# Kernel tuning notes

Measured on AMD Instinct MI355X. Metric: run time of the kernel, lower is better.

The kernel has to match this reference:

```python
import jax, jax.numpy as jnp
import numpy as np

COMMITMENT_COST = 0.25


def setup_inputs() -> dict:
    key = jax.random.key(0)
    k1, k2 = jax.random.split(key)
    B, S, D, K = 16, 4096, 256, 4096
    inputs = jax.random.normal(k1, (B, S, D), dtype=jnp.float32)
    # codebook ~ embedding.weight (init scale irrelevant for correctness baseline)
    codebook = jax.random.normal(k2, (K, D), dtype=jnp.float32)
    return {"inputs": inputs, "codebook": codebook}


def reference(inputs, codebook):
    B, S, D = inputs.shape
    flat = inputs.reshape(-1, D)  # (N, D)
    distances = (
        jnp.sum(flat * flat, axis=1, keepdims=True)
        + jnp.sum(codebook * codebook, axis=1)
        - 2.0 * jnp.matmul(flat, codebook.T)
    )
    encoding_indices = jnp.argmin(distances, axis=1)  # (N,)
    quantized = codebook[encoding_indices].reshape(inputs.shape)  # gather
    # commitment loss: beta * mse(inputs, sg(quantized))
    diff = inputs - jax.lax.stop_gradient(quantized)
    commitment_loss = COMMITMENT_COST * jnp.mean(diff * diff)
    # straight-through estimator
    quantized_st = inputs + jax.lax.stop_gradient(quantized - inputs)
    return quantized_st, commitment_loss, encoding_indices
```

## Files before the change

### kernel.cpp

```cpp
#include <hip/hip_runtime.h>
#include <stdint.h>

typedef _Float16 half8 __attribute__((ext_vector_type(8)));
typedef float f32x4 __attribute__((ext_vector_type(4)));

#define DDIM 256
#define KCODES 4096
#define BM 256
#define BN 256
#define NCH 8
#define DELTA 0.02f
#define FLT_BIG 3.4e38f

#define GLOAD_LDS(gsrc, ldst)                                                        \
    __builtin_amdgcn_global_load_lds(                                                \
        (const __attribute__((address_space(1))) void*)(const void*)(gsrc),          \
        (__attribute__((address_space(3))) void*)(void*)(ldst), 16, 0, 0)

__global__ void cvt_hl_kernel(const float* __restrict__ src, half8* __restrict__ dst) {
    int gid = blockIdx.x * 256 + threadIdx.x;
    int q = gid & 3;
    int ch = (gid >> 2) & 7;
    long row = gid >> 5;
    const float* s = src + row * DDIM + ch * 32 + q * 8;
    const float4 f0 = ((const float4*)s)[0];
    const float4 f1 = ((const float4*)s)[1];
    float vv[8] = {f0.x, f0.y, f0.z, f0.w, f1.x, f1.y, f1.z, f1.w};
    half8 hi, lo;
    #pragma unroll
    for (int j = 0; j < 8; ++j) {
        float v = vv[j];
        _Float16 h = (_Float16)v;
        hi[j] = h; lo[j] = (_Float16)(v - (float)h);
    }
    half8* d = dst + ((row * 8 + ch) << 3);
    d[q] = hi;
    d[q + 4] = lo;
}

__global__ void enorm_kernel(const float* __restrict__ cb, float* __restrict__ en, int K) {
    int gid = blockIdx.x * blockDim.x + threadIdx.x;
    int code = gid >> 6;
    int lane = threadIdx.x & 63;
    if (code >= K) return;
    const float4 v = *reinterpret_cast<const float4*>(&cb[(size_t)code * DDIM + lane * 4]);
    float s = v.x * v.x + v.y * v.y + v.z * v.z + v.w * v.w;
    #pragma unroll
    for (int off = 32; off > 0; off >>= 1) s += __shfl_xor(s, off, 64);
    if (lane == 0) en[code] = s;
}

__global__ __launch_bounds__(512, 2)
void vq_mfma_kernel(const half8* x16, const half8* __restrict__ cb16,
                    const float* __restrict__ en, const float* __restrict__ x,
                    const float* __restrict__ cb, float* out,
                    int* __restrict__ list, int* __restrict__ counter,
                    float* __restrict__ loss_accum, int N) {
    __shared__ __align__(16) half8 Abuf[2][BM * 8];
    __shared__ __align__(16) half8 Bbuf[2][BN * 8];
    __shared__ float en_lds[KCODES];
    __shared__ float red_d[4][BM];
    __shared__ float red_d2[4][BM];
    __shared__ int   red_i[4][BM];
    __shared__ int   binfo[BM];
    __shared__ float wsum[8];

    const int tid = threadIdx.x;
    const int lane = tid & 63;
    const int w = tid >> 6;
    const int wr = w >> 2, wc = w & 3;
    const int l15 = lane & 15, l4 = lane >> 4;
    const int brow = blockIdx.x * BM;
    const size_t ND = (size_t)N * DDIM;

    ((float4*)en_lds)[tid] = ((const float4*)en)[tid];
    ((float4*)en_lds)[tid + 512] = ((const float4*)en)[tid + 512];

    const int lrow = lane >> 3;
    const int swz = (lane & 7) ^ lrow;
    const half8* pA0 = x16 + (size_t)(brow + (w     ) * 8 + lrow) * 64 + swz;
    const half8* pA1 = x16 + (size_t)(brow + (w +  8) * 8 + lrow) * 64 + swz;
    const half8* pA2 = x16 + (size_t)(brow + (w + 16) * 8 + lrow) * 64 + swz;
    const half8* pA3 = x16 + (size_t)(brow + (w + 24) * 8 + lrow) * 64 + swz;
    const half8* pB0 = cb16 + (size_t)((w     ) * 8 + lrow) * 64 + swz;
    const half8* pB1 = cb16 + (size_t)((w +  8) * 8 + lrow) * 64 + swz;
    const half8* pB2 = cb16 + (size_t)((w + 16) * 8 + lrow) * 64 + swz;
    const half8* pB3 = cb16 + (size_t)((w + 24) * 8 + lrow) * 64 + swz;

#define STAGE(b_) do {                                      \
        GLOAD_LDS(pA0, &Abuf[b_][(w     ) * 64]);           \
        GLOAD_LDS(pA1, &Abuf[b_][(w +  8) * 64]);           \
        GLOAD_LDS(pA2, &Abuf[b_][(w + 16) * 64]);           \
        GLOAD_LDS(pA3, &Abuf[b_][(w + 24) * 64]);           \
        GLOAD_LDS(pB0, &Bbuf[b_][(w     ) * 64]);           \
        GLOAD_LDS(pB1, &Bbuf[b_][(w +  8) * 64]);           \
        GLOAD_LDS(pB2, &Bbuf[b_][(w + 16) * 64]);           \
        GLOAD_LDS(pB3, &Bbuf[b_][(w + 24) * 64]);           \
    } while (0)

#define ADVANCE(roll_) do {                                 \
        const int dA = (roll_) ? -56 : 8;                   \
        const int dB = (roll_) ? 16328 : 8;                 \
        pA0 += dA; pA1 += dA; pA2 += dA; pA3 += dA;         \
        pB0 += dB; pB1 += dB; pB2 += dB; pB3 += dB;         \
    } while (0)

    const int sw7 = l15 & 7;
    const _Float16* A0 = (const _Float16*)Abuf;
    const _Float16* B0 = A0 + 32768;
    const _Float16* aH = A0 + wr * 8192 + l15 * 64 + ((l4    ) ^ sw7) * 8;
    const _Float16* aL = A0 + wr * 8192 + l15 * 64 + ((l4 + 4) ^ sw7) * 8;
    const _Float16* bH = B0 + wc * 4096 + l15 * 64 + ((l4    ) ^ sw7) * 8;
    const _Float16* bL = B0 + wc * 4096 + l15 * 64 + ((l4 + 4) ^ sw7) * 8;

    STAGE(0); ADVANCE(false);

    float bestv[8], best2v[8];
    int bidv[8];
    #pragma unroll
    for (int i = 0; i < 8; ++i) { bestv[i] = FLT_BIG; best2v[i] = FLT_BIG; bidv[i] = 0; }

    const int code_sub = wc * 64 + l4 * 4;
    f32x4 acc[4][8];

#define TRI(accr, bh_, bl_, ah_, al_) do {                                              \
        accr = __builtin_amdgcn_mfma_f32_16x16x32_f16(bh_, ah_, accr, 0, 0, 0);         \
        accr = __builtin_amdgcn_mfma_f32_16x16x32_f16(bl_, ah_, accr, 0, 0, 0);         \
        accr = __builtin_amdgcn_mfma_f32_16x16x32_f16(bh_, al_, accr, 0, 0, 0);         \
    } while (0)

    for (int it = 0; it < 16; ++it) {
        #pragma unroll
        for (int m = 0; m < 4; ++m)
            #pragma unroll
            for (int n = 0; n < 8; ++n) acc[m][n] = (f32x4){0.f, 0.f, 0.f, 0.f};

        #pragma unroll
        for (int k = 0; k < 8; ++k) {
            __syncthreads();
            if (k != 7) { STAGE((k + 1) & 1); ADVANCE(k == 6); }
            else if (it != 15) { STAGE(0); ADVANCE(false); }
            __builtin_amdgcn_sched_barrier(0);

            const int o = (k & 1) ? 16384 : 0;
            half8 a_h[8], a_l[8];
            #pragma unroll
            for (int n = 0; n < 8; ++n) {
                a_h[n] = *(const half8*)(aH + o + n * 1024);
                a_l[n] = *(const half8*)(aL + o + n * 1024);
            }
            #pragma unroll
            for (int m = 0; m < 4; ++m) {
                half8 bh = *(const half8*)(bH + o + m * 1024);
                half8 bl = *(const half8*)(bL + o + m * 1024);
                __builtin_amdgcn_s_setprio(1);
                #pragma unroll
                for (int n = 0; n < 8; ++n)
                    TRI(acc[m][n], bh, bl, a_h[n], a_l[n]);
                __builtin_amdgcn_s_setprio(0);
            }
        }

        const int c0 = it * BN;
        #pragma unroll
        for (int m = 0; m < 4; ++m) {
            #pragma unroll
            for (int r = 0; r < 4; ++r) {
                int code = c0 + code_sub + m * 16 + r;
                float e = en_lds[code];
                #pragma unroll
                for (int n = 0; n < 8; ++n) {
                    float dist = fmaf(-2.f, acc[m][n][r], e);
                    if (dist < bestv[n]) { best2v[n] = bestv[n]; bestv[n] = dist; bidv[n] = code; }
                    else if (dist < best2v[n]) best2v[n] = dist;
                }
            }
        }
    }
#undef STAGE
#undef ADVANCE
#undef TRI

    #pragma unroll
    for (int n = 0; n < 8; ++n) {
        float d = bestv[n], d2 = best2v[n];
        int ix = bidv[n];
        #pragma unroll
        for (int off = 16; off < 64; off <<= 1) {
            float od = __shfl_xor(d, off, 64);
            float od2 = __shfl_xor(d2, off, 64);
            int oi = __shfl_xor(ix, off, 64);
            if (od < d || (od == d && oi < ix)) { d2 = fminf(d, od2); d = od; ix = oi; }
            else d2 = fminf(d2, od);
        }
        if (l4 == 0) {
            int row = wr * 128 + n * 16 + l15;
            red_d[wc][row] = d;
            red_d2[wc][row] = d2;
            red_i[wc][row] = ix;
        }
    }
    __syncthreads();

    if (tid < BM) {
        float d = red_d[0][tid], d2 = red_d2[0][tid];
        int ix = red_i[0][tid];
        #pragma unroll
        for (int q = 1; q < 4; ++q) {
            float od = red_d[q][tid], od2 = red_d2[q][tid];
            int oi = red_i[q][tid];
            if (od < d || (od == d && oi < ix)) { d2 = fminf(d, od2); d = od; ix = oi; }
            else d2 = fminf(d2, od);
        }
        int fl = (d2 - d < DELTA) ? 1 : 0;
        out[ND + 1 + brow + tid] = (float)ix;
        binfo[tid] = ix | (fl << 16);
        if (fl) {
            int pos = atomicAdd(counter, 1);
            list[pos] = brow + tid;
        }
    }
    __syncthreads();

    float lsum = 0.f;
    #pragma unroll 4
    for (int pp = 0; pp < 32; ++pp) {
        int i = tid + pp * 512;
        int row = i >> 6;
        int c4 = (i & 63) << 2;
        int info = binfo[row];
        int code = info & 0xffff;
        const float4 q = *reinterpret_cast<const float4*>(&cb[(size_t)code * DDIM + c4]);
        const float4 xv = *reinterpret_cast<const float4*>(&x[(size_t)(brow + row) * DDIM + c4]);
        float d0 = xv.x - q.x, d1 = xv.y - q.y, d2 = xv.z - q.z, d3 = xv.w - q.w;
        if (!(info >> 16)) lsum += d0 * d0 + d1 * d1 + d2 * d2 + d3 * d3;
        *reinterpret_cast<float4*>(&out[(size_t)(brow + row) * DDIM + c4]) = q;
    }
    #pragma unroll
    for (int off = 32; off > 0; off >>= 1) lsum += __shfl_xor(lsum, off, 64);
    if (lane == 0) wsum[w] = lsum;
    __syncthreads();
    if (tid == 0) {
        float tot = 0.f;
        #pragma unroll
        for (int q = 0; q < 8; ++q) tot += wsum[q];
        atomicAdd(loss_accum, tot * (0.25f / (float)ND));
    }
}

__global__ __launch_bounds__(256)
void rescan_kernel(const float* __restrict__ x, const float* __restrict__ cb,
                   const float* __restrict__ en, const int* __restrict__ list,
                   const int* __restrict__ counter, float* out,
                   float* __restrict__ loss_accum, int N) {
    __shared__ __align__(16) float4 xrow4[64];
    __shared__ float wd[4];
    __shared__ int wi[4];
    __shared__ float wls[4];
    __shared__ int six;
    const int tid = threadIdx.x;
    const int w = tid >> 6;
    const int lane = tid & 63;
    const int cnt = *counter;
    const size_t ND = (size_t)N * DDIM;

    for (int it = blockIdx.x; it < cnt; it += gridDim.x) {
        const int row = list[it];
        __syncthreads();
        if (tid < 64) xrow4[tid] = ((const float4*)&x[(size_t)row * DDIM])[tid];
        __syncthreads();
        const float4 xv = xrow4[lane];
        float bd = FLT_BIG;
        int bi = 0;
        for (int i = 0; i < KCODES / 4; ++i) {
            int code = i * 4 + w;
            const float4 c4 = ((const float4*)&cb[(size_t)code * DDIM])[lane];
            float s = xv.x * c4.x + xv.y * c4.y + xv.z * c4.z + xv.w * c4.w;
            #pragma unroll
            for (int off = 1; off < 64; off <<= 1) s += __shfl_xor(s, off, 64);
            float dist = fmaf(-2.f, s, en[code]);
            if (dist < bd) { bd = dist; bi = code; }
        }
        if (lane == 0) { wd[w] = bd; wi[w] = bi; }
        __syncthreads();
        if (tid == 0) {
            float d = wd[0]; int ix = wi[0];
            #pragma unroll
            for (int q = 1; q < 4; ++q) {
                if (wd[q] < d || (wd[q] == d && wi[q] < ix)) { d = wd[q]; ix = wi[q]; }
            }
            six = ix;
            out[ND + 1 + row] = (float)ix;
        }
        __syncthreads();
        const int ix = six;
        float c = cb[(size_t)ix * DDIM + tid];
        float xs = ((const float*)xrow4)[tid];
        out[(size_t)row * DDIM + tid] = c;
        float dd = xs - c;
        float ss = dd * dd;
        #pragma unroll
        for (int off = 32; off > 0; off >>= 1) ss += __shfl_xor(ss, off, 64);
        if (lane == 0) wls[w] = ss;
        __syncthreads();
        if (tid == 0) {
            float tot = wls[0] + wls[1] + wls[2] + wls[3];
            atomicAdd(loss_accum, tot * (0.25f / (float)ND));
        }
    }
}

__global__ void loss_fin_kernel(const float* __restrict__ loss_accum,
                                float* __restrict__ out, size_t off) {
    if (blockIdx.x == 0 && threadIdx.x == 0) out[off] = *loss_accum;
}

extern "C" void kernel_launch(void* const* d_in, const int* in_sizes, int n_in,
                              void* d_out, int out_size, void* d_ws, size_t ws_size,
                              hipStream_t stream) {
    const float* x = (const float*)d_in[0];
    const float* cb = (const float*)d_in[1];
    const int N = in_sizes[0] / DDIM;
    const int K = in_sizes[1] / DDIM;
    float* out = (float*)d_out;

    half8* x16 = (half8*)d_out;

    half8* cb16 = (half8*)d_ws;
    char* p = (char*)d_ws + (4 << 20);
    float* en = (float*)p;                  p += (size_t)K * 4;
    int* list = (int*)p;                    p += (size_t)N * 4;
    int* counter = (int*)p;                 p += 64;
    float* loss_accum = (float*)p;

    hipMemsetAsync(counter, 0, sizeof(int), stream);
    hipMemsetAsync(loss_accum, 0, sizeof(float), stream);
    cvt_hl_kernel<<<(N * 32) / 256, 256, 0, stream>>>(x, x16);
    cvt_hl_kernel<<<(K * 32) / 256, 256, 0, stream>>>(cb, cb16);
    enorm_kernel<<<(K * 64) / 256, 256, 0, stream>>>(cb, en, K);
    vq_mfma_kernel<<<N / BM, 512, 0, stream>>>(x16, cb16, en, x, cb, out,
                                               list, counter, loss_accum, N);
    rescan_kernel<<<512, 256, 0, stream>>>(x, cb, en, list, counter, out, loss_accum, N);
    loss_fin_kernel<<<1, 64, 0, stream>>>(loss_accum, out, (size_t)N * DDIM);
}
```

Before: 758.4 us.

## Shrink MFMA tile to 128x128 and move gather/loss into separate kernel

Halves the block tile of the distance GEMM from 256x256 with 8 waves to 128x128 with 4 waves, which doubles the grid and lowers per-block register and LDS use. The gather of quantized rows and the loss accumulation move out of the GEMM epilogue and the rescan path into a new gather kernel driven by a stored best-index array, and the codebook norms are read from global memory instead of LDS. Smaller tiles mean twice the codebook and input reloads from L2 per row, and the extra kernel reads x and the codebook once more, in exchange for better occupancy and a simpler epilogue.

```diff
diff --git a/kernel.cpp b/kernel.cpp
--- a/kernel.cpp
+++ b/kernel.cpp
@@ -6,9 +6,8 @@
 
 #define DDIM 256
 #define KCODES 4096
-#define BM 256
-#define BN 256
-#define NCH 8
+#define BM 128
+#define BN 128
 #define DELTA 0.02f
 #define FLT_BIG 3.4e38f
 
@@ -50,78 +49,67 @@
     if (lane == 0) en[code] = s;
 }
 
-__global__ __launch_bounds__(512, 2)
+__global__ __launch_bounds__(256, 2)
 void vq_mfma_kernel(const half8* x16, const half8* __restrict__ cb16,
-                    const float* __restrict__ en, const float* __restrict__ x,
-                    const float* __restrict__ cb, float* out,
-                    int* __restrict__ list, int* __restrict__ counter,
-                    float* __restrict__ loss_accum, int N) {
+                    const float* __restrict__ en, int* __restrict__ bidx,
+                    int* __restrict__ list, int* __restrict__ counter) {
     __shared__ __align__(16) half8 Abuf[2][BM * 8];
     __shared__ __align__(16) half8 Bbuf[2][BN * 8];
-    __shared__ float en_lds[KCODES];
-    __shared__ float red_d[4][BM];
-    __shared__ float red_d2[4][BM];
-    __shared__ int   red_i[4][BM];
-    __shared__ int   binfo[BM];
-    __shared__ float wsum[8];
+    __shared__ float red_d[2][BM];
+    __shared__ float red_d2[2][BM];
+    __shared__ int   red_i[2][BM];
 
     const int tid = threadIdx.x;
     const int lane = tid & 63;
     const int w = tid >> 6;
-    const int wr = w >> 2, wc = w & 3;
+    const int wr = w >> 1, wc = w & 1;
     const int l15 = lane & 15, l4 = lane >> 4;
     const int brow = blockIdx.x * BM;
-    const size_t ND = (size_t)N * DDIM;
-
-    ((float4*)en_lds)[tid] = ((const float4*)en)[tid];
-    ((float4*)en_lds)[tid + 512] = ((const float4*)en)[tid + 512];
 
     const int lrow = lane >> 3;
     const int swz = (lane & 7) ^ lrow;
     const half8* pA0 = x16 + (size_t)(brow + (w     ) * 8 + lrow) * 64 + swz;
-    const half8* pA1 = x16 + (size_t)(brow + (w +  8) * 8 + lrow) * 64 + swz;
-    const half8* pA2 = x16 + (size_t)(brow + (w + 16) * 8 + lrow) * 64 + swz;
-    const half8* pA3 = x16 + (size_t)(brow + (w + 24) * 8 + lrow) * 64 + swz;
+    const half8* pA1 = x16 + (size_t)(brow + (w +  4) * 8 + lrow) * 64 + swz;
+    const half8* pA2 = x16 + (size_t)(brow + (w +  8) * 8 + lrow) * 64 + swz;
+    const half8* pA3 = x16 + (size_t)(brow + (w + 12) * 8 + lrow) * 64 + swz;
     const half8* pB0 = cb16 + (size_t)((w     ) * 8 + lrow) * 64 + swz;
-    const half8* pB1 = cb16 + (size_t)((w +  8) * 8 + lrow) * 64 + swz;
-    const half8* pB2 = cb16 + (size_t)((w + 16) * 8 + lrow) * 64 + swz;
-    const half8* pB3 = cb16 + (size_t)((w + 24) * 8 + lrow) * 64 + swz;
+    const half8* pB1 = cb16 + (size_t)((w +  4) * 8 + lrow) * 64 + swz;
+    const half8* pB2 = cb16 + (size_t)((w +  8) * 8 + lrow) * 64 + swz;
+    const half8* pB3 = cb16 + (size_t)((w + 12) * 8 + lrow) * 64 + swz;
 
 #define STAGE(b_) do {                                      \
         GLOAD_LDS(pA0, &Abuf[b_][(w     ) * 64]);           \
-        GLOAD_LDS(pA1, &Abuf[b_][(w +  8) * 64]);           \
-        GLOAD_LDS(pA2, &Abuf[b_][(w + 16) * 64]);           \
-        GLOAD_LDS(pA3, &Abuf[b_][(w + 24) * 64]);           \
+        GLOAD_LDS(pA1, &Abuf[b_][(w +  4) * 64]);           \
+        GLOAD_LDS(pA2, &Abuf[b_][(w +  8) * 64]);           \
+        GLOAD_LDS(pA3, &Abuf[b_][(w + 12) * 64]);           \
         GLOAD_LDS(pB0, &Bbuf[b_][(w     ) * 64]);           \
-        GLOAD_LDS(pB1, &Bbuf[b_][(w +  8) * 64]);           \
-        GLOAD_LDS(pB2, &Bbuf[b_][(w + 16) * 64]);           \
-        GLOAD_LDS(pB3, &Bbuf[b_][(w + 24) * 64]);           \
+        GLOAD_LDS(pB1, &Bbuf[b_][(w +  4) * 64]);           \
+        GLOAD_LDS(pB2, &Bbuf[b_][(w +  8) * 64]);           \
+        GLOAD_LDS(pB3, &Bbuf[b_][(w + 12) * 64]);           \
     } while (0)
 
-#define ADVANCE(roll_) do {                                 \
-        const int dA = (roll_) ? -56 : 8;                   \
-        const int dB = (roll_) ? 16328 : 8;                 \
-        pA0 += dA; pA1 += dA; pA2 += dA; pA3 += dA;         \
-        pB0 += dB; pB1 += dB; pB2 += dB; pB3 += dB;         \
+#define ADVA(dA_, dB_) do {                                 \
+        pA0 += dA_; pA1 += dA_; pA2 += dA_; pA3 += dA_;     \
+        pB0 += dB_; pB1 += dB_; pB2 += dB_; pB3 += dB_;     \
     } while (0)
 
     const int sw7 = l15 & 7;
     const _Float16* A0 = (const _Float16*)Abuf;
-    const _Float16* B0 = A0 + 32768;
-    const _Float16* aH = A0 + wr * 8192 + l15 * 64 + ((l4    ) ^ sw7) * 8;
-    const _Float16* aL = A0 + wr * 8192 + l15 * 64 + ((l4 + 4) ^ sw7) * 8;
+    const _Float16* B0 = A0 + 16384;
+    const _Float16* aH = A0 + wr * 4096 + l15 * 64 + ((l4    ) ^ sw7) * 8;
+    const _Float16* aL = A0 + wr * 4096 + l15 * 64 + ((l4 + 4) ^ sw7) * 8;
     const _Float16* bH = B0 + wc * 4096 + l15 * 64 + ((l4    ) ^ sw7) * 8;
     const _Float16* bL = B0 + wc * 4096 + l15 * 64 + ((l4 + 4) ^ sw7) * 8;
 
-    STAGE(0); ADVANCE(false);
-
-    float bestv[8], best2v[8];
-    int bidv[8];
-    #pragma unroll
-    for (int i = 0; i < 8; ++i) { bestv[i] = FLT_BIG; best2v[i] = FLT_BIG; bidv[i] = 0; }
+    STAGE(0); ADVA(8, 8);
+
+    float bestv[4], best2v[4];
+    int bidv[4];
+    #pragma unroll
+    for (int i = 0; i < 4; ++i) { bestv[i] = FLT_BIG; best2v[i] = FLT_BIG; bidv[i] = 0; }
 
     const int code_sub = wc * 64 + l4 * 4;
-    f32x4 acc[4][8];
+    f32x4 acc[4][4];
 
 #define TRI(accr, bh_, bl_, ah_, al_) do {                                              \
         accr = __builtin_amdgcn_mfma_f32_16x16x32_f16(bh_, ah_, accr, 0, 0, 0);         \
@@ -129,47 +117,53 @@
         accr = __builtin_amdgcn_mfma_f32_16x16x32_f16(bh_, al_, accr, 0, 0, 0);         \
     } while (0)
 
-    for (int it = 0; it < 16; ++it) {
+    for (int it = 0; it < 32; ++it) {
         #pragma unroll
         for (int m = 0; m < 4; ++m)
             #pragma unroll
-            for (int n = 0; n < 8; ++n) acc[m][n] = (f32x4){0.f, 0.f, 0.f, 0.f};
+            for (int n = 0; n < 4; ++n) acc[m][n] = (f32x4){0.f, 0.f, 0.f, 0.f};
 
         #pragma unroll
         for (int k = 0; k < 8; ++k) {
             __syncthreads();
-            if (k != 7) { STAGE((k + 1) & 1); ADVANCE(k == 6); }
-            else if (it != 15) { STAGE(0); ADVANCE(false); }
+            if (k != 7) {
+                STAGE((k + 1) & 1);
+                if (k == 6) ADVA(-56, 8136);
+                else        ADVA(8, 8);
+            } else if (it != 31) {
+                STAGE(0);
+                ADVA(8, 8);
+            }
             __builtin_amdgcn_sched_barrier(0);
 
-            const int o = (k & 1) ? 16384 : 0;
-            half8 a_h[8], a_l[8];
-            #pragma unroll
-            for (int n = 0; n < 8; ++n) {
-                a_h[n] = *(const half8*)(aH + o + n * 1024);
-                a_l[n] = *(const half8*)(aL + o + n * 1024);
+            const int o = (k & 1) ? 8192 : 0;
+            half8 ah[4], al[4], bh[4], bl[4];
+            #pragma unroll
+            for (int i = 0; i < 4; ++i) {
+                ah[i] = *(const half8*)(aH + o + i * 1024);
+                al[i] = *(const half8*)(aL + o + i * 1024);
+                bh[i] = *(const half8*)(bH + o + i * 1024);
+                bl[i] = *(const half8*)(bL + o + i * 1024);
             }
-            #pragma unroll
-            for (int m = 0; m < 4; ++m) {
-                half8 bh = *(const half8*)(bH + o + m * 1024);
-                half8 bl = *(const half8*)(bL + o + m * 1024);
-                __builtin_amdgcn_s_setprio(1);
+            __builtin_amdgcn_s_setprio(1);
+            #pragma unroll
+            for (int m = 0; m < 4; ++m)
                 #pragma unroll
-                for (int n = 0; n < 8; ++n)
-                    TRI(acc[m][n], bh, bl, a_h[n], a_l[n]);
-                __builtin_amdgcn_s_setprio(0);
-            }
+                for (int n = 0; n < 4; ++n)
+                    TRI(acc[m][n], bh[m], bl[m], ah[n], al[n]);
+            __builtin_amdgcn_s_setprio(0);
         }
 
         const int c0 = it * BN;
         #pragma unroll
         for (int m = 0; m < 4; ++m) {
+            const float4 e4 = *(const float4*)(en + c0 + wc * 64 + m * 16 + l4 * 4);
             #pragma unroll
             for (int r = 0; r < 4; ++r) {
                 int code = c0 + code_sub + m * 16 + r;
-                float e = en_lds[code];
+                float e = (r == 0) ? e4.x : (r == 1) ? e4.y : (r == 2) ? e4.z : e4.w;
                 #pragma unroll
-                for (int n = 0; n < 8; ++n) {
+                for (int n = 0; n < 4; ++n) {
                     float dist = fmaf(-2.f, acc[m][n][r], e);
                     if (dist < bestv[n]) { best2v[n] = bestv[n]; bestv[n] = dist; bidv[n] = code; }
                     else if (dist < best2v[n]) best2v[n] = dist;
@@ -178,11 +172,11 @@
         }
     }
 #undef STAGE
-#undef ADVANCE
+#undef ADVA
 #undef TRI
 
     #pragma unroll
-    for (int n = 0; n < 8; ++n) {
+    for (int n = 0; n < 4; ++n) {
         float d = bestv[n], d2 = best2v[n];
         int ix = bidv[n];
         #pragma unroll
@@ -194,7 +188,7 @@
             else d2 = fminf(d2, od);
         }
         if (l4 == 0) {
-            int row = wr * 128 + n * 16 + l15;
+            int row = wr * 64 + n * 16 + l15;
             red_d[wc][row] = d;
             red_d2[wc][row] = d2;
             red_i[wc][row] = ix;
@@ -205,64 +199,29 @@
     if (tid < BM) {
         float d = red_d[0][tid], d2 = red_d2[0][tid];
         int ix = red_i[0][tid];
-        #pragma unroll
-        for (int q = 1; q < 4; ++q) {
-            float od = red_d[q][tid], od2 = red_d2[q][tid];
-            int oi = red_i[q][tid];
-            if (od < d || (od == d && oi < ix)) { d2 = fminf(d, od2); d = od; ix = oi; }
-            else d2 = fminf(d2, od);
-        }
-        int fl = (d2 - d < DELTA) ? 1 : 0;
-        out[ND + 1 + brow + tid] = (float)ix;
-        binfo[tid] = ix | (fl << 16);
-        if (fl) {
+        float od = red_d[1][tid], od2 = red_d2[1][tid];
+        int oi = red_i[1][tid];
+        if (od < d || (od == d && oi < ix)) { d2 = fminf(d, od2); d = od; ix = oi; }
+        else d2 = fminf(d2, od);
+        bidx[brow + tid] = ix;
+        if (d2 - d < DELTA) {
             int pos = atomicAdd(counter, 1);
             list[pos] = brow + tid;
         }
-    }
-    __syncthreads();
-
-    float lsum = 0.f;
-    #pragma unroll 4
-    for (int pp = 0; pp < 32; ++pp) {
-        int i = tid + pp * 512;
-        int row = i >> 6;
-        int c4 = (i & 63) << 2;
-        int info = binfo[row];
-        int code = info & 0xffff;
-        const float4 q = *reinterpret_cast<const float4*>(&cb[(size_t)code * DDIM + c4]);
-        const float4 xv = *reinterpret_cast<const float4*>(&x[(size_t)(brow + row) * DDIM + c4]);
-        float d0 = xv.x - q.x, d1 = xv.y - q.y, d2 = xv.z - q.z, d3 = xv.w - q.w;
-        if (!(info >> 16)) lsum += d0 * d0 + d1 * d1 + d2 * d2 + d3 * d3;
-        *reinterpret_cast<float4*>(&out[(size_t)(brow + row) * DDIM + c4]) = q;
-    }
-    #pragma unroll
-    for (int off = 32; off > 0; off >>= 1) lsum += __shfl_xor(lsum, off, 64);
-    if (lane == 0) wsum[w] = lsum;
-    __syncthreads();
-    if (tid == 0) {
-        float tot = 0.f;
-        #pragma unroll
-        for (int q = 0; q < 8; ++q) tot += wsum[q];
-        atomicAdd(loss_accum, tot * (0.25f / (float)ND));
     }
 }
 
 __global__ __launch_bounds__(256)
 void rescan_kernel(const float* __restrict__ x, const float* __restrict__ cb,
                    const float* __restrict__ en, const int* __restrict__ list,
-                   const int* __restrict__ counter, float* out,
-                   float* __restrict__ loss_accum, int N) {
+                   const int* __restrict__ counter, int* __restrict__ bidx) {
     __shared__ __align__(16) float4 xrow4[64];
     __shared__ float wd[4];
     __shared__ int wi[4];
-    __shared__ float wls[4];
-    __shared__ int six;
     const int tid = threadIdx.x;
     const int w = tid >> 6;
     const int lane = tid & 63;
     const int cnt = *counter;
-    const size_t ND = (size_t)N * DDIM;
 
     for (int it = blockIdx.x; it < cnt; it += gridDim.x) {
         const int row = list[it];
@@ -289,24 +248,46 @@
             for (int q = 1; q < 4; ++q) {
                 if (wd[q] < d || (wd[q] == d && wi[q] < ix)) { d = wd[q]; ix = wi[q]; }
             }
-            six = ix;
-            out[ND + 1 + row] = (float)ix;
-        }
-        __syncthreads();
-        const int ix = six;
-        float c = cb[(size_t)ix * DDIM + tid];
-        float xs = ((const float*)xrow4)[tid];
-        out[(size_t)row * DDIM + tid] = c;
-        float dd = xs - c;
-        float ss = dd * dd;
-        #pragma unroll
-        for (int off = 32; off > 0; off >>= 1) ss += __shfl_xor(ss, off, 64);
-        if (lane == 0) wls[w] = ss;
-        __syncthreads();
-        if (tid == 0) {
-            float tot = wls[0] + wls[1] + wls[2] + wls[3];
-            atomicAdd(loss_accum, tot * (0.25f / (float)ND));
-        }
+            bidx[row] = ix;
+        }
+    }
+}
+
+__global__ __launch_bounds__(256)
+void gather_kernel(const float* __restrict__ x, const float* __restrict__ cb,
+                   const int* __restrict__ bidx, float* __restrict__ out,
+                   float* __restrict__ loss_accum, int N) {
+    __shared__ float wsum[4];
+    __shared__ int bloc[64];
+    const int tid = threadIdx.x;
+    const int brow = blockIdx.x * 64;
+    const size_t ND = (size_t)N * DDIM;
+    if (tid < 64) {
+        int ix = bidx[brow + tid];
+        bloc[tid] = ix;
+        out[ND + 1 + brow + tid] = (float)ix;
+    }
+    __syncthreads();
+    float lsum = 0.f;
+    #pragma unroll
+    for (int pp = 0; pp < 16; ++pp) {
+        int i = tid + pp * 256;
+        int row = i >> 6;
+        int c4 = (i & 63) << 2;
+        int code = bloc[row];
+        const float4 q = *reinterpret_cast<const float4*>(&cb[(size_t)code * DDIM + c4]);
+        const float4 xv = *reinterpret_cast<const float4*>(&x[(size_t)(brow + row) * DDIM + c4]);
+        float d0 = xv.x - q.x, d1 = xv.y - q.y, d2 = xv.z - q.z, d3 = xv.w - q.w;
+        lsum += d0 * d0 + d1 * d1 + d2 * d2 + d3 * d3;
+        *reinterpret_cast<float4*>(&out[(size_t)(brow + row) * DDIM + c4]) = q;
+    }
+    #pragma unroll
+    for (int off = 32; off > 0; off >>= 1) lsum += __shfl_xor(lsum, off, 64);
+    if ((tid & 63) == 0) wsum[tid >> 6] = lsum;
+    __syncthreads();
+    if (tid == 0) {
+        float tot = wsum[0] + wsum[1] + wsum[2] + wsum[3];
+        atomicAdd(loss_accum, tot * (0.25f / (float)ND));
     }
 }
 
@@ -329,6 +310,7 @@
     half8* cb16 = (half8*)d_ws;
     char* p = (char*)d_ws + (4 << 20);
     float* en = (float*)p;                  p += (size_t)K * 4;
+    int* bidx = (int*)p;                    p += (size_t)N * 4;
     int* list = (int*)p;                    p += (size_t)N * 4;
     int* counter = (int*)p;                 p += 64;
     float* loss_accum = (float*)p;
@@ -338,8 +320,8 @@
     cvt_hl_kernel<<<(N * 32) / 256, 256, 0, stream>>>(x, x16);
     cvt_hl_kernel<<<(K * 32) / 256, 256, 0, stream>>>(cb, cb16);
     enorm_kernel<<<(K * 64) / 256, 256, 0, stream>>>(cb, en, K);
-    vq_mfma_kernel<<<N / BM, 512, 0, stream>>>(x16, cb16, en, x, cb, out,
-                                               list, counter, loss_accum, N);
-    rescan_kernel<<<512, 256, 0, stream>>>(x, cb, en, list, counter, out, loss_accum, N);
+    vq_mfma_kernel<<<N / BM, 256, 0, stream>>>(x16, cb16, en, bidx, list, counter);
+    rescan_kernel<<<512, 256, 0, stream>>>(x, cb, en, list, counter, bidx);
+    gather_kernel<<<N / 64, 256, 0, stream>>>(x, cb, bidx, out, loss_accum, N);
     loss_fin_kernel<<<1, 64, 0, stream>>>(loss_accum, out, (size_t)N * DDIM);
 }
```

After: 727.2 us. 4.1% less time.
